# Kernel optimization log

Hardware: AMD Instinct MI355X
Metric: run time of the kernel (lower is better)

The kernel has to match this reference:

```python
import jax, jax.numpy as jnp
from jax import lax
import numpy as np

B, T, IN, H, OUT = 8192, 512, 8, 64, 1


def setup_inputs() -> dict:
    key = jax.random.key(0)
    ks = jax.random.split(key, 7)
    s_ih = 1.0 / np.sqrt(H)
    # PyTorch LSTM param layout: gates stacked as [i, f, g, o] along dim 0
    W_ih = jax.random.uniform(ks[0], (4 * H, IN), jnp.float32, -s_ih, s_ih)
    W_hh = jax.random.uniform(ks[1], (4 * H, H), jnp.float32, -s_ih, s_ih)
    b_ih = jax.random.uniform(ks[2], (4 * H,), jnp.float32, -s_ih, s_ih)
    b_hh = jax.random.uniform(ks[3], (4 * H,), jnp.float32, -s_ih, s_ih)
    W_fc = jax.random.uniform(ks[4], (OUT, H), jnp.float32, -s_ih, s_ih)
    b_fc = jax.random.uniform(ks[5], (OUT,), jnp.float32, -s_ih, s_ih)
    x = jax.random.normal(ks[6], (B, T, IN), jnp.float32)
    return {"x": x, "W_ih": W_ih, "W_hh": W_hh, "b_ih": b_ih,
            "b_hh": b_hh, "W_fc": W_fc, "b_fc": b_fc}


def _lstm_last_h(x, W_ih, W_hh, b_ih, b_hh):
    # x: [B, T, IN] -> last hidden state [B, H]
    Bn = x.shape[0]
    Hn = W_hh.shape[1]
    b = b_ih + b_hh  # [4H]

    def step(carry, xt):
        h, c = carry  # [B, H] each
        gates = xt @ W_ih.T + h @ W_hh.T + b  # [B, 4H]
        i, f, g, o = jnp.split(gates, 4, axis=-1)
        i = jax.nn.sigmoid(i)
        f = jax.nn.sigmoid(f)
        g = jnp.tanh(g)
        o = jax.nn.sigmoid(o)
        c = f * c + i * g
        h = o * jnp.tanh(c)
        return (h, c), None

    h0 = jnp.zeros((Bn, Hn), x.dtype)
    c0 = jnp.zeros((Bn, Hn), x.dtype)
    (hT, _), _ = lax.scan(step, (h0, c0), jnp.swapaxes(x, 0, 1))  # scan over T
    return hT


def reference(x, W_ih, W_hh, b_ih, b_hh, W_fc, b_fc):
    hT = _lstm_last_h(x, W_ih, W_hh, b_ih, b_hh)  # [B, H]
    return hT @ W_fc.T + b_fc  # [B, OUT]
```

## Files before the change

### kernel.cpp

```cpp
#include <hip/hip_runtime.h>


typedef _Float16 f16_t;
typedef _Float16 half8 __attribute__((ext_vector_type(8)));
typedef _Float16 half4 __attribute__((ext_vector_type(4)));
typedef __fp16 fp16x2 __attribute__((ext_vector_type(2)));
typedef float floatx2 __attribute__((ext_vector_type(2)));
typedef float floatx4 __attribute__((ext_vector_type(4)));

#define Bn 8192
#define Tn 512
#define INn 8
#define Hn 64
#define BT 16
#define CHUNK 16
#define NCHUNK (Tn / CHUNK)
#define HSTRIDE 72
#define XROW 24

__device__ __forceinline__ floatx2 act_pair(float zi0, float zi1,
                                            float zf0, float zf1,
                                            float zg0, float zg1,
                                            float zo0, float zo1,
                                            floatx2& chat) {
  const floatx2 one  = {1.f, 1.f};
  const float  K2   = 2.8853900817779268f;
  const floatx2 K2v  = {K2, K2};
  const floatx2 mK2v = {-K2, -K2};
  const floatx2 clmp = {126.f, 126.f};
  floatx2 A = {__builtin_amdgcn_exp2f(zi0), __builtin_amdgcn_exp2f(zi1)};
  floatx2 G = {__builtin_amdgcn_exp2f(zg0), __builtin_amdgcn_exp2f(zg1)};
  floatx2 F = {__builtin_amdgcn_exp2f(zf0), __builtin_amdgcn_exp2f(zf1)};
  floatx2 O = {__builtin_amdgcn_exp2f(zo0), __builtin_amdgcn_exp2f(zo1)};
  floatx2 PA  = A + one;
  floatx2 PG  = G + one;
  floatx2 PF  = F + one;
  floatx2 PAG = PA * PG;
  floatx2 num = __builtin_elementwise_fma(G, K2v, mK2v) * PF;
  floatx2 s   = __builtin_elementwise_fma(chat, PAG, num);
  floatx2 P3  = PF * PAG;
  {
    const float r3 = __builtin_amdgcn_rcpf(P3.x * P3.y);
    const floatx2 r3v = {r3, r3};
    const floatx2 P3s = {P3.y, P3.x};
    chat = __builtin_elementwise_min(s * (r3v * P3s), clmp);
  }
  floatx2 C2 = {__builtin_amdgcn_exp2f(chat.x), __builtin_amdgcn_exp2f(chat.y)};
  floatx2 P4 = (O + one) * (C2 + one);
  {
    const float r4 = __builtin_amdgcn_rcpf(P4.x * P4.y);
    const floatx2 r4v = {r4, r4};
    const floatx2 P4s = {P4.y, P4.x};
    return (C2 - one) * (r4v * P4s);
  }
}

__global__ __launch_bounds__(256, 2)
void lstm_fused(const float* __restrict__ xg,
                const float* __restrict__ W_ih,
                const float* __restrict__ W_hh,
                const float* __restrict__ b_ih,
                const float* __restrict__ b_hh,
                const float* __restrict__ W_fc,
                const float* __restrict__ b_fc,
                float* __restrict__ out)
{
  __shared__ alignas(16) f16_t hbuf[2][BT][HSTRIDE];
  __shared__ alignas(16) f16_t xlds[2][CHUNK][BT][XROW];

  const int tid   = threadIdx.x;
  const int wv    = tid >> 6;
  const int lane  = tid & 63;
  const int n     = lane & 15;
  const int q     = lane >> 4;
  const int bbase = blockIdx.x * BT;

  const float LOG2E = 1.4426950408889634f;

  half8 bf[4][2];
  half4 bfx[4];
  #pragma unroll
  for (int g = 0; g < 4; ++g) {
    const float sc = (g == 2) ? (2.f * LOG2E) : (-LOG2E);
    const int C = g * 64 + wv * 16 + n;
    #pragma unroll
    for (int c = 0; c < 2; ++c) {
      half8 v;
      #pragma unroll
      for (int j = 0; j < 8; ++j) {
        const int k = c * 32 + q * 8 + j;
        v[j] = (f16_t)(W_hh[C * Hn + k] * sc);
      }
      bf[g][c] = v;
    }
    half4 vx;
    #pragma unroll
    for (int j = 0; j < 4; ++j) {
      const int k = q * 4 + j;
      vx[j] = (f16_t)((k < INn) ? (W_ih[C * INn + k] * sc) : 0.f);
    }
    bfx[g] = vx;
  }

  const int u0 = wv * 16 + q * 4;
  floatx4 bi, bfv, bg, bo;
  #pragma unroll
  for (int r = 0; r < 4; ++r) {
    const int uu = u0 + r;
    bi[r]  = -(b_ih[uu]        + b_hh[uu])        * LOG2E;
    bfv[r] = -(b_ih[64 + uu]   + b_hh[64 + uu])   * LOG2E;
    bg[r]  =  (b_ih[128 + uu]  + b_hh[128 + uu])  * (2.f * LOG2E);
    bo[r]  = -(b_ih[192 + uu]  + b_hh[192 + uu])  * LOG2E;
  }

  const int row_s = tid >> 4;
  const int tt_s  = tid & 15;
  const float* xps = xg + ((size_t)(bbase + row_s) * Tn + tt_s) * INn;

  for (int i = tid; i < BT * HSTRIDE; i += 256) ((f16_t*)hbuf[0])[i] = (f16_t)0.f;
  {
    const half8 z = {};
    #pragma unroll
    for (int r = tid; r < 2 * CHUNK * BT; r += 256) {
      f16_t* base = &xlds[r >> 8][(r >> 4) & 15][r & 15][0];
      *(half8*)(base + 8)  = z;
      *(half8*)(base + 16) = z;
    }
  }
  {
    float4 a  = *(const float4*)(xps);
    float4 b2 = *(const float4*)(xps + 4);
    union { half8 v; fp16x2 h2[4]; } P;
    P.h2[0] = __builtin_amdgcn_cvt_pkrtz(a.x, a.y);
    P.h2[1] = __builtin_amdgcn_cvt_pkrtz(a.z, a.w);
    P.h2[2] = __builtin_amdgcn_cvt_pkrtz(b2.x, b2.y);
    P.h2[3] = __builtin_amdgcn_cvt_pkrtz(b2.z, b2.w);
    *(half8*)&xlds[0][tt_s][row_s][0] = P.v;
  }
  float4 pa  = *(const float4*)(xps + CHUNK * INn);
  float4 pb2 = *(const float4*)(xps + CHUNK * INn + 4);

  __syncthreads();

  floatx2 chat01 = {0.f, 0.f};
  floatx2 chat23 = {0.f, 0.f};

  for (int ch = 0; ch < NCHUNK; ++ch) {
    half4 bx[CHUNK];
    #pragma unroll
    for (int t = 0; t < CHUNK; ++t)
      bx[t] = *(const half4*)&xlds[ch & 1][t][n][q * 4];

    #pragma unroll
    for (int tt = 0; tt < CHUNK; ++tt) {
      const int p  = tt & 1;
      const int pn = p ^ 1;

      const half8 b0 = *(const half8*)&hbuf[p][n][q * 8];
      const half8 b1 = *(const half8*)&hbuf[p][n][32 + q * 8];

      __builtin_amdgcn_s_setprio(1);
      floatx4 ai = __builtin_amdgcn_mfma_f32_16x16x32_f16(bf[0][0], b0, bi,  0, 0, 0);
      floatx4 af = __builtin_amdgcn_mfma_f32_16x16x32_f16(bf[1][0], b0, bfv, 0, 0, 0);
      floatx4 ag = __builtin_amdgcn_mfma_f32_16x16x32_f16(bf[2][0], b0, bg,  0, 0, 0);
      floatx4 ao = __builtin_amdgcn_mfma_f32_16x16x32_f16(bf[3][0], b0, bo,  0, 0, 0);
      ai = __builtin_amdgcn_mfma_f32_16x16x32_f16(bf[0][1], b1, ai, 0, 0, 0);
      af = __builtin_amdgcn_mfma_f32_16x16x32_f16(bf[1][1], b1, af, 0, 0, 0);
      ag = __builtin_amdgcn_mfma_f32_16x16x32_f16(bf[2][1], b1, ag, 0, 0, 0);
      ao = __builtin_amdgcn_mfma_f32_16x16x32_f16(bf[3][1], b1, ao, 0, 0, 0);
      ai = __builtin_amdgcn_mfma_f32_16x16x16f16(bfx[0], bx[tt], ai, 0, 0, 0);
      af = __builtin_amdgcn_mfma_f32_16x16x16f16(bfx[1], bx[tt], af, 0, 0, 0);
      ag = __builtin_amdgcn_mfma_f32_16x16x16f16(bfx[2], bx[tt], ag, 0, 0, 0);
      ao = __builtin_amdgcn_mfma_f32_16x16x16f16(bfx[3], bx[tt], ao, 0, 0, 0);
      __builtin_amdgcn_s_setprio(0);

      if (tt == 0) {
        union { half8 v; fp16x2 h2[4]; } P;
        P.h2[0] = __builtin_amdgcn_cvt_pkrtz(pa.x, pa.y);
        P.h2[1] = __builtin_amdgcn_cvt_pkrtz(pa.z, pa.w);
        P.h2[2] = __builtin_amdgcn_cvt_pkrtz(pb2.x, pb2.y);
        P.h2[3] = __builtin_amdgcn_cvt_pkrtz(pb2.z, pb2.w);
        *(half8*)&xlds[(ch + 1) & 1][tt_s][row_s][0] = P.v;
      }
      if (tt == 1) {
        const int chn = (ch + 2 < NCHUNK) ? (ch + 2) : (ch + 2 - NCHUNK);
        pa  = *(const float4*)(xps + (size_t)chn * CHUNK * INn);
        pb2 = *(const float4*)(xps + (size_t)chn * CHUNK * INn + 4);
      }

      const floatx2 h01 = act_pair(ai[0], ai[1], af[0], af[1],
                                   ag[0], ag[1], ao[0], ao[1], chat01);
      const floatx2 h23 = act_pair(ai[2], ai[3], af[2], af[3],
                                   ag[2], ag[3], ao[2], ao[3], chat23);

      union { half4 v; fp16x2 h2[2]; } Wq;
      Wq.h2[0] = __builtin_amdgcn_cvt_pkrtz(h01.x, h01.y);
      Wq.h2[1] = __builtin_amdgcn_cvt_pkrtz(h23.x, h23.y);
      *(half4*)&hbuf[pn][n][u0] = Wq.v;

      __syncthreads();
    }
  }

  if (tid < 64) {
    const int b = lane & 15;
    const int part = lane >> 4;
    float s = 0.f;
    #pragma unroll
    for (int k = 0; k < 16; ++k) {
      const int uu = part * 16 + k;
      s = __builtin_fmaf((float)hbuf[0][b][uu], W_fc[uu], s);
    }
    s += __shfl_down(s, 32);
    s += __shfl_down(s, 16);
    if (lane < 16) out[bbase + b] = s + b_fc[0];
  }
}

extern "C" void kernel_launch(void* const* d_in, const int* in_sizes, int n_in,
                              void* d_out, int out_size, void* d_ws, size_t ws_size,
                              hipStream_t stream) {
  const float* x    = (const float*)d_in[0];
  const float* W_ih = (const float*)d_in[1];
  const float* W_hh = (const float*)d_in[2];
  const float* b_ih = (const float*)d_in[3];
  const float* b_hh = (const float*)d_in[4];
  const float* W_fc = (const float*)d_in[5];
  const float* b_fc = (const float*)d_in[6];
  float* out = (float*)d_out;
  dim3 grid(Bn / BT), block(256);
  hipLaunchKernelGGL(lstm_fused, grid, block, 0, stream,
                     x, W_ih, W_hh, b_ih, b_hh, W_fc, b_fc, out);
}
```

Before: 437.4 us.

## Split gate work across eight waves with interleaved gate-row layout

Doubles the block to eight waves so each wave owns eight hidden units, and reorders the weight rows so each MFMA output row holds all four gates of one unit. Each wave then issues six MFMAs per step instead of twelve and evaluates a single activation pair, which shortens the serial per-step critical path of the recurrence. In exchange every step's barrier now spans eight waves, the h stores become scalar 16-bit LDS writes, and occupancy drops to four resident waves... per SIMD at the requested bounds; only the first 256 threads stage x.

```diff
diff --git a/kernel.cpp b/kernel.cpp
--- a/kernel.cpp
+++ b/kernel.cpp
@@ -13,6 +13,8 @@
 #define INn 8
 #define Hn 64
 #define BT 16
+#define NW 8
+#define NTHR (NW * 64)
 #define CHUNK 16
 #define NCHUNK (Tn / CHUNK)
 #define HSTRIDE 72
@@ -55,7 +57,7 @@
   }
 }
 
-__global__ __launch_bounds__(256, 2)
+__global__ __launch_bounds__(NTHR, 4)
 void lstm_fused(const float* __restrict__ xg,
                 const float* __restrict__ W_ih,
                 const float* __restrict__ W_hh,
@@ -77,12 +79,14 @@
 
   const float LOG2E = 1.4426950408889634f;
 
-  half8 bf[4][2];
-  half4 bfx[4];
+  half8 bf[2][2];
+  half4 bfx[2];
   #pragma unroll
-  for (int g = 0; g < 4; ++g) {
-    const float sc = (g == 2) ? (2.f * LOG2E) : (-LOG2E);
-    const int C = g * 64 + wv * 16 + n;
+  for (int T = 0; T < 2; ++T) {
+    const int gate = n & 3;
+    const int unit = 8 * wv + 4 * T + (n >> 2);
+    const float sc = (gate == 2) ? (2.f * LOG2E) : (-LOG2E);
+    const int C = gate * 64 + unit;
     #pragma unroll
     for (int c = 0; c < 2; ++c) {
       half8 v;
@@ -91,7 +95,7 @@
         const int k = c * 32 + q * 8 + j;
         v[j] = (f16_t)(W_hh[C * Hn + k] * sc);
       }
-      bf[g][c] = v;
+      bf[T][c] = v;
     }
     half4 vx;
     #pragma unroll
@@ -99,35 +103,36 @@
       const int k = q * 4 + j;
       vx[j] = (f16_t)((k < INn) ? (W_ih[C * INn + k] * sc) : 0.f);
     }
-    bfx[g] = vx;
-  }
-
-  const int u0 = wv * 16 + q * 4;
-  floatx4 bi, bfv, bg, bo;
+    bfx[T] = vx;
+  }
+
+  floatx4 bias[2];
   #pragma unroll
-  for (int r = 0; r < 4; ++r) {
-    const int uu = u0 + r;
-    bi[r]  = -(b_ih[uu]        + b_hh[uu])        * LOG2E;
-    bfv[r] = -(b_ih[64 + uu]   + b_hh[64 + uu])   * LOG2E;
-    bg[r]  =  (b_ih[128 + uu]  + b_hh[128 + uu])  * (2.f * LOG2E);
-    bo[r]  = -(b_ih[192 + uu]  + b_hh[192 + uu])  * LOG2E;
-  }
-
-  const int row_s = tid >> 4;
+  for (int T = 0; T < 2; ++T) {
+    const int uT = 8 * wv + 4 * T + q;
+    bias[T][0] = -(b_ih[uT]        + b_hh[uT])        * LOG2E;
+    bias[T][1] = -(b_ih[64 + uT]   + b_hh[64 + uT])   * LOG2E;
+    bias[T][2] =  (b_ih[128 + uT]  + b_hh[128 + uT])  * (2.f * LOG2E);
+    bias[T][3] = -(b_ih[192 + uT]  + b_hh[192 + uT])  * LOG2E;
+  }
+  const int uA = 8 * wv + q;
+  const int uB = 8 * wv + 4 + q;
+
+  const int row_s = (tid >> 4) & 15;
   const int tt_s  = tid & 15;
   const float* xps = xg + ((size_t)(bbase + row_s) * Tn + tt_s) * INn;
 
-  for (int i = tid; i < BT * HSTRIDE; i += 256) ((f16_t*)hbuf[0])[i] = (f16_t)0.f;
+  for (int i = tid; i < BT * HSTRIDE; i += NTHR) ((f16_t*)hbuf[0])[i] = (f16_t)0.f;
   {
     const half8 z = {};
-    #pragma unroll
-    for (int r = tid; r < 2 * CHUNK * BT; r += 256) {
+    for (int r = tid; r < 2 * CHUNK * BT; r += NTHR) {
       f16_t* base = &xlds[r >> 8][(r >> 4) & 15][r & 15][0];
       *(half8*)(base + 8)  = z;
       *(half8*)(base + 16) = z;
     }
   }
-  {
+  float4 pa = {}, pb2 = {};
+  if (tid < 256) {
     float4 a  = *(const float4*)(xps);
     float4 b2 = *(const float4*)(xps + 4);
     union { half8 v; fp16x2 h2[4]; } P;
@@ -136,14 +141,13 @@
     P.h2[2] = __builtin_amdgcn_cvt_pkrtz(b2.x, b2.y);
     P.h2[3] = __builtin_amdgcn_cvt_pkrtz(b2.z, b2.w);
     *(half8*)&xlds[0][tt_s][row_s][0] = P.v;
-  }
-  float4 pa  = *(const float4*)(xps + CHUNK * INn);
-  float4 pb2 = *(const float4*)(xps + CHUNK * INn + 4);
+    pa  = *(const float4*)(xps + CHUNK * INn);
+    pb2 = *(const float4*)(xps + CHUNK * INn + 4);
+  }
 
   __syncthreads();
 
-  floatx2 chat01 = {0.f, 0.f};
-  floatx2 chat23 = {0.f, 0.f};
+  floatx2 chat = {0.f, 0.f};
 
   for (int ch = 0; ch < NCHUNK; ++ch) {
     half4 bx[CHUNK];
@@ -160,21 +164,15 @@
       const half8 b1 = *(const half8*)&hbuf[p][n][32 + q * 8];
 
       __builtin_amdgcn_s_setprio(1);
-      floatx4 ai = __builtin_amdgcn_mfma_f32_16x16x32_f16(bf[0][0], b0, bi,  0, 0, 0);
-      floatx4 af = __builtin_amdgcn_mfma_f32_16x16x32_f16(bf[1][0], b0, bfv, 0, 0, 0);
-      floatx4 ag = __builtin_amdgcn_mfma_f32_16x16x32_f16(bf[2][0], b0, bg,  0, 0, 0);
-      floatx4 ao = __builtin_amdgcn_mfma_f32_16x16x32_f16(bf[3][0], b0, bo,  0, 0, 0);
-      ai = __builtin_amdgcn_mfma_f32_16x16x32_f16(bf[0][1], b1, ai, 0, 0, 0);
-      af = __builtin_amdgcn_mfma_f32_16x16x32_f16(bf[1][1], b1, af, 0, 0, 0);
-      ag = __builtin_amdgcn_mfma_f32_16x16x32_f16(bf[2][1], b1, ag, 0, 0, 0);
-      ao = __builtin_amdgcn_mfma_f32_16x16x32_f16(bf[3][1], b1, ao, 0, 0, 0);
-      ai = __builtin_amdgcn_mfma_f32_16x16x16f16(bfx[0], bx[tt], ai, 0, 0, 0);
-      af = __builtin_amdgcn_mfma_f32_16x16x16f16(bfx[1], bx[tt], af, 0, 0, 0);
-      ag = __builtin_amdgcn_mfma_f32_16x16x16f16(bfx[2], bx[tt], ag, 0, 0, 0);
-      ao = __builtin_amdgcn_mfma_f32_16x16x16f16(bfx[3], bx[tt], ao, 0, 0, 0);
+      floatx4 a1 = __builtin_amdgcn_mfma_f32_16x16x32_f16(bf[0][0], b0, bias[0], 0, 0, 0);
+      floatx4 a2 = __builtin_amdgcn_mfma_f32_16x16x32_f16(bf[1][0], b0, bias[1], 0, 0, 0);
+      a1 = __builtin_amdgcn_mfma_f32_16x16x32_f16(bf[0][1], b1, a1, 0, 0, 0);
+      a2 = __builtin_amdgcn_mfma_f32_16x16x32_f16(bf[1][1], b1, a2, 0, 0, 0);
+      a1 = __builtin_amdgcn_mfma_f32_16x16x16f16(bfx[0], bx[tt], a1, 0, 0, 0);
+      a2 = __builtin_amdgcn_mfma_f32_16x16x16f16(bfx[1], bx[tt], a2, 0, 0, 0);
       __builtin_amdgcn_s_setprio(0);
 
-      if (tt == 0) {
+      if (tt == 0 && tid < 256) {
         union { half8 v; fp16x2 h2[4]; } P;
         P.h2[0] = __builtin_amdgcn_cvt_pkrtz(pa.x, pa.y);
         P.h2[1] = __builtin_amdgcn_cvt_pkrtz(pa.z, pa.w);
@@ -182,21 +180,16 @@
         P.h2[3] = __builtin_amdgcn_cvt_pkrtz(pb2.z, pb2.w);
         *(half8*)&xlds[(ch + 1) & 1][tt_s][row_s][0] = P.v;
       }
-      if (tt == 1) {
+      if (tt == 1 && tid < 256) {
         const int chn = (ch + 2 < NCHUNK) ? (ch + 2) : (ch + 2 - NCHUNK);
         pa  = *(const float4*)(xps + (size_t)chn * CHUNK * INn);
         pb2 = *(const float4*)(xps + (size_t)chn * CHUNK * INn + 4);
       }
 
-      const floatx2 h01 = act_pair(ai[0], ai[1], af[0], af[1],
-                                   ag[0], ag[1], ao[0], ao[1], chat01);
-      const floatx2 h23 = act_pair(ai[2], ai[3], af[2], af[3],
-                                   ag[2], ag[3], ao[2], ao[3], chat23);
-
-      union { half4 v; fp16x2 h2[2]; } Wq;
-      Wq.h2[0] = __builtin_amdgcn_cvt_pkrtz(h01.x, h01.y);
-      Wq.h2[1] = __builtin_amdgcn_cvt_pkrtz(h23.x, h23.y);
-      *(half4*)&hbuf[pn][n][u0] = Wq.v;
+      const floatx2 h = act_pair(a1[0], a2[0], a1[1], a2[1],
+                                 a1[2], a2[2], a1[3], a2[3], chat);
+      hbuf[pn][n][uA] = (f16_t)h.x;
+      hbuf[pn][n][uB] = (f16_t)h.y;
 
       __syncthreads();
     }
@@ -228,7 +221,7 @@
   const float* W_fc = (const float*)d_in[5];
   const float* b_fc = (const float*)d_in[6];
   float* out = (float*)d_out;
-  dim3 grid(Bn / BT), block(256);
+  dim3 grid(Bn / BT), block(NTHR);
   hipLaunchKernelGGL(lstm_fused, grid, block, 0, stream,
                      x, W_ih, W_hh, b_ih, b_hh, W_fc, b_fc, out);
 }
```

New measurement: 445.6 us. About the same (+1.9%).
